# Optimization experiments

Measured on AMD Instinct MI355X. Metric: run time of the kernel, lower is better.

The kernel has to match this reference:

```python
import jax, jax.numpy as jnp
import numpy as np

FILLER = 10.1  # filler_value from __init__
B, C, L, KEEP = 128, 16, 16384, 12288


def setup_inputs() -> dict:
    key = jax.random.key(0)
    k1, k2, k3, k4 = jax.random.split(key, 4)
    x1 = jax.random.normal(k1, (B, C, 4096), dtype=jnp.float32)
    x2 = jax.random.normal(k2, (B, C, 4096), dtype=jnp.float32)
    x3 = jax.random.normal(k3, (B, C, L), dtype=jnp.float32)
    # Scatter exactly (L - KEEP) filler entries at random positions in every row,
    # so per-row compaction yields a uniform length KEEP (required by np.stack
    # in the original module).
    u = jax.random.uniform(k4, (B, C, L))
    ranks = jnp.argsort(jnp.argsort(u, axis=-1), axis=-1)  # random permutation ranks
    fill_mask = ranks < (L - KEEP)
    x3 = jnp.where(fill_mask, jnp.float32(FILLER), x3)
    return {"x1": x1, "x2": x2, "x3": x3, "keep_len": KEEP}


def reference(x1, x2, x3, keep_len):
    # Per-row stream compaction: drop entries equal to FILLER, keep original
    # order of survivors, output fixed length keep_len.
    is_filler = x3 == jnp.float32(FILLER)          # [B, C, L] bool
    # Stable argsort moves non-filler (False=0) to the front, order-preserving.
    order = jnp.argsort(is_filler, axis=-1, stable=True)  # [B, C, L]
    compacted = jnp.take_along_axis(x3, order, axis=-1)    # [B, C, L]
    return compacted[..., :keep_len]                        # [B, C, keep_len]
```

## Files before the change

### kernel.cpp

```cpp
#include <hip/hip_runtime.h>


#define FILLER_VAL 10.1f
constexpr int L_LEN    = 16384;
constexpr int KEEP_LEN = 12288;
constexpr int WAVE     = 64;
constexpr int CHUNK    = WAVE * 4;
constexpr int CPR      = L_LEN / CHUNK;
constexpr int PF       = 8;
constexpr int RING     = 2048;
constexpr int RM       = RING - 1;
constexpr int FLUSH_Q  = 256;

__device__ __forceinline__ int lane_prefix(unsigned long long m)
{
    return __builtin_amdgcn_mbcnt_hi((unsigned)(m >> 32),
           __builtin_amdgcn_mbcnt_lo((unsigned)m, 0u));
}

__global__ __launch_bounds__(WAVE, 4) void compact_rows_kernel(
    const float* __restrict__ x3, float* __restrict__ out)
{
    const int row  = blockIdx.x;
    const int lane = threadIdx.x;
    const float* __restrict__ in = x3 + (size_t)row * L_LEN;
    float* __restrict__ o = out + (size_t)row * KEEP_LEN;

    __shared__ float ring[RING];

    float4 buf[PF];
    #pragma unroll
    for (int i = 0; i < PF; ++i)
        buf[i] = *reinterpret_cast<const float4*>(in + i * CHUNK + lane * 4);

    int rowoff  = 0;
    int flushed = 0;

    #pragma unroll 1
    for (int g = 0; g < CPR / PF; ++g) {
        #pragma unroll
        for (int s = 0; s < PF; ++s) {
            const int c = g * PF + s;
            const float4 v = buf[s];
            if (c + PF < CPR)
                buf[s] = *reinterpret_cast<const float4*>(
                    in + (c + PF) * CHUNK + lane * 4);

            const bool kx = (v.x != FILLER_VAL);
            const bool ky = (v.y != FILLER_VAL);
            const bool kz = (v.z != FILLER_VAL);
            const bool kw = (v.w != FILLER_VAL);
            const unsigned long long m0 = __ballot(kx);
            const unsigned long long m1 = __ballot(ky);
            const unsigned long long m2 = __ballot(kz);
            const unsigned long long m3 = __ballot(kw);

            const int before = lane_prefix(m0) + lane_prefix(m1)
                             + lane_prefix(m2) + lane_prefix(m3);
            const int p0 = rowoff + before;
            const int p1 = p0 + (int)kx;
            const int p2 = p1 + (int)ky;
            const int p3 = p2 + (int)kz;
            if (kx) ring[p0 & RM] = v.x;
            if (ky) ring[p1 & RM] = v.y;
            if (kz) ring[p2 & RM] = v.z;
            if (kw) ring[p3 & RM] = v.w;

            rowoff += __popcll(m0) + __popcll(m1)
                    + __popcll(m2) + __popcll(m3);

            while (rowoff - flushed >= FLUSH_Q) {
                const int rbase = (flushed & RM) + lane * 4;
                const float4 t = *reinterpret_cast<const float4*>(&ring[rbase]);
                if (flushed < KEEP_LEN)
                    *reinterpret_cast<float4*>(&o[flushed + lane * 4]) = t;
                flushed += FLUSH_Q;
            }
        }
    }

    const int rem = rowoff - flushed;
    #pragma unroll
    for (int j = 0; j < 4; ++j) {
        const int i = lane * 4 + j;
        if (i < rem && flushed + i < KEEP_LEN)
            o[flushed + i] = ring[(flushed + i) & RM];
    }
}

extern "C" void kernel_launch(void* const* d_in, const int* in_sizes, int n_in,
                              void* d_out, int out_size, void* d_ws, size_t ws_size,
                              hipStream_t stream)
{
    const float* x3 = (const float*)d_in[2];
    float* out = (float*)d_out;

    const int rows = in_sizes[2] / L_LEN;

    compact_rows_kernel<<<rows, WAVE, 0, stream>>>(x3, out);
}
```

Before: 256.7 us.

## Split row compaction into count pass and segment-parallel compact pass

Adds a counting kernel that computes per-segment survivor counts, then a compaction kernel where four waves each handle a quarter of a row using prefix offsets from those counts. This raises parallelism from one wave per row to four, targeting latency-bound execution. It costs an extra full read of the input and a second launch, and output writes become scalar and unaligned.

```diff
diff --git a/kernel.cpp b/kernel.cpp
--- a/kernel.cpp
+++ b/kernel.cpp
@@ -4,13 +4,16 @@
 #define FILLER_VAL 10.1f
 constexpr int L_LEN    = 16384;
 constexpr int KEEP_LEN = 12288;
+constexpr int SEGS     = 4;
+constexpr int SEG_LEN  = L_LEN / SEGS;
 constexpr int WAVE     = 64;
+constexpr int BLOCK    = 256;
 constexpr int CHUNK    = WAVE * 4;
-constexpr int CPR      = L_LEN / CHUNK;
+constexpr int CPS      = SEG_LEN / CHUNK;
 constexpr int PF       = 8;
-constexpr int RING     = 2048;
+constexpr int RING     = 1024;
 constexpr int RM       = RING - 1;
-constexpr int FLUSH_Q  = 256;
+constexpr int FQ       = 256;
 
 __device__ __forceinline__ int lane_prefix(unsigned long long m)
 {
@@ -18,33 +21,69 @@
            __builtin_amdgcn_mbcnt_lo((unsigned)m, 0u));
 }
 
-__global__ __launch_bounds__(WAVE, 4) void compact_rows_kernel(
-    const float* __restrict__ x3, float* __restrict__ out)
+__global__ __launch_bounds__(BLOCK, 8) void count_kernel(
+    const float* __restrict__ x3, int* __restrict__ cnt)
 {
     const int row  = blockIdx.x;
-    const int lane = threadIdx.x;
-    const float* __restrict__ in = x3 + (size_t)row * L_LEN;
+    const int lane = threadIdx.x & 63;
+    const int w    = threadIdx.x >> 6;
+    const float* __restrict__ s = x3 + (size_t)row * L_LEN + w * SEG_LEN;
+
+    int total = 0;
+    #pragma unroll 1
+    for (int half = 0; half < CPS / PF; ++half) {
+        float4 buf[PF];
+        #pragma unroll
+        for (int i = 0; i < PF; ++i)
+            buf[i] = *reinterpret_cast<const float4*>(
+                s + (half * PF + i) * CHUNK + lane * 4);
+        #pragma unroll
+        for (int i = 0; i < PF; ++i) {
+            total += __popcll(__ballot(buf[i].x != FILLER_VAL))
+                   + __popcll(__ballot(buf[i].y != FILLER_VAL))
+                   + __popcll(__ballot(buf[i].z != FILLER_VAL))
+                   + __popcll(__ballot(buf[i].w != FILLER_VAL));
+        }
+    }
+    if (lane == 0) cnt[row * SEGS + w] = total;
+}
+
+__global__ __launch_bounds__(BLOCK, 6) void compact_kernel(
+    const float* __restrict__ x3, const int* __restrict__ cnt,
+    float* __restrict__ out)
+{
+    const int row  = blockIdx.x;
+    const int lane = threadIdx.x & 63;
+    const int w    = threadIdx.x >> 6;
+    const float* __restrict__ s = x3 + (size_t)row * L_LEN + w * SEG_LEN;
     float* __restrict__ o = out + (size_t)row * KEEP_LEN;
 
-    __shared__ float ring[RING];
+    __shared__ float ring[SEGS][RING];
+    float* r = ring[w];
+
+    const int4 c4 = *reinterpret_cast<const int4*>(cnt + row * SEGS);
+    int base = 0;
+    if (w > 0) base += c4.x;
+    if (w > 1) base += c4.y;
+    if (w > 2) base += c4.z;
 
     float4 buf[PF];
     #pragma unroll
     for (int i = 0; i < PF; ++i)
-        buf[i] = *reinterpret_cast<const float4*>(in + i * CHUNK + lane * 4);
+        buf[i] = *reinterpret_cast<const float4*>(s + i * CHUNK + lane * 4);
 
-    int rowoff  = 0;
-    int flushed = 0;
+    int off = 0;
+    int fl  = 0;
 
     #pragma unroll 1
-    for (int g = 0; g < CPR / PF; ++g) {
+    for (int g = 0; g < CPS / PF; ++g) {
         #pragma unroll
-        for (int s = 0; s < PF; ++s) {
-            const int c = g * PF + s;
-            const float4 v = buf[s];
-            if (c + PF < CPR)
-                buf[s] = *reinterpret_cast<const float4*>(
-                    in + (c + PF) * CHUNK + lane * 4);
+        for (int sN = 0; sN < PF; ++sN) {
+            const int c = g * PF + sN;
+            const float4 v = buf[sN];
+            if (c + PF < CPS)
+                buf[sN] = *reinterpret_cast<const float4*>(
+                    s + (c + PF) * CHUNK + lane * 4);
 
             const bool kx = (v.x != FILLER_VAL);
             const bool ky = (v.y != FILLER_VAL);
@@ -57,34 +96,38 @@
 
             const int before = lane_prefix(m0) + lane_prefix(m1)
                              + lane_prefix(m2) + lane_prefix(m3);
-            const int p0 = rowoff + before;
+            const int p0 = off + before;
             const int p1 = p0 + (int)kx;
             const int p2 = p1 + (int)ky;
             const int p3 = p2 + (int)kz;
-            if (kx) ring[p0 & RM] = v.x;
-            if (ky) ring[p1 & RM] = v.y;
-            if (kz) ring[p2 & RM] = v.z;
-            if (kw) ring[p3 & RM] = v.w;
+            if (kx) r[p0 & RM] = v.x;
+            if (ky) r[p1 & RM] = v.y;
+            if (kz) r[p2 & RM] = v.z;
+            if (kw) r[p3 & RM] = v.w;
 
-            rowoff += __popcll(m0) + __popcll(m1)
-                    + __popcll(m2) + __popcll(m3);
+            off += __popcll(m0) + __popcll(m1)
+                 + __popcll(m2) + __popcll(m3);
 
-            while (rowoff - flushed >= FLUSH_Q) {
-                const int rbase = (flushed & RM) + lane * 4;
-                const float4 t = *reinterpret_cast<const float4*>(&ring[rbase]);
-                if (flushed < KEEP_LEN)
-                    *reinterpret_cast<float4*>(&o[flushed + lane * 4]) = t;
-                flushed += FLUSH_Q;
+            while (off - fl >= FQ) {
+                #pragma unroll
+                for (int i = 0; i < FQ / WAVE; ++i) {
+                    const int li = fl + i * WAVE + lane;
+                    const float t = r[li & RM];
+                    const int gp = base + li;
+                    if (gp < KEEP_LEN) o[gp] = t;
+                }
+                fl += FQ;
             }
         }
     }
 
-    const int rem = rowoff - flushed;
     #pragma unroll
-    for (int j = 0; j < 4; ++j) {
-        const int i = lane * 4 + j;
-        if (i < rem && flushed + i < KEEP_LEN)
-            o[flushed + i] = ring[(flushed + i) & RM];
+    for (int i = 0; i < FQ / WAVE; ++i) {
+        const int li = fl + i * WAVE + lane;
+        if (li < off) {
+            const int gp = base + li;
+            if (gp < KEEP_LEN) o[gp] = r[li & RM];
+        }
     }
 }
 
@@ -94,8 +137,10 @@
 {
     const float* x3 = (const float*)d_in[2];
     float* out = (float*)d_out;
+    int* cnt = (int*)d_ws;
 
     const int rows = in_sizes[2] / L_LEN;
 
-    compact_rows_kernel<<<rows, WAVE, 0, stream>>>(x3, out);
+    count_kernel<<<rows, BLOCK, 0, stream>>>(x3, cnt);
+    compact_kernel<<<rows, BLOCK, 0, stream>>>(x3, cnt, out);
 }
```

After: 275.2 us. 7.2% more time.
